# Performance work log

Hardware: AMD Instinct MI355X
Metric: run time of the kernel (lower is better)

## Reference

```python
import jax, jax.numpy as jnp
import numpy as np

N_NODES = 50000
N_EDGES = 800000
NEG_SLOPE = 0.2  # PyG GATConv default


def _gat_layer(x, src, dst, n, W, a_src, a_dst, b, concat):
    """One GATConv layer (PyG semantics, eval mode so attention dropout is off).

    x: [N, F_in], src/dst: [E'] (self loops included), W: [F_in, H*C],
    a_src/a_dst: [H, C], b: [H*C] if concat else [C].
    """
    H, C = a_src.shape
    h = (x @ W).reshape(n, H, C)                      # [N, H, C]
    al_s = jnp.sum(h * a_src, axis=-1)                # [N, H]
    al_d = jnp.sum(h * a_dst, axis=-1)                # [N, H]
    e = jax.nn.leaky_relu(al_s[src] + al_d[dst], NEG_SLOPE)  # [E', H]
    # numerically stable softmax over incoming edges of each dst node
    m = jax.lax.stop_gradient(jax.ops.segment_max(e, dst, num_segments=n))
    m = jnp.where(jnp.isfinite(m), m, 0.0)
    ex = jnp.exp(e - m[dst])                          # [E', H]
    denom = jax.ops.segment_sum(ex, dst, num_segments=n)     # [N, H]
    alpha = ex / denom[dst]                           # safe: self loops => denom > 0
    out = jax.ops.segment_sum(alpha[:, :, None] * h[src], dst, num_segments=n)  # [N,H,C]
    out = out.reshape(n, H * C) if concat else out.mean(axis=1)
    return out + b


def setup_inputs() -> dict:
    key = jax.random.key(0)
    ks = jax.random.split(key, 8)
    in_dim, hid, heads, out_dim = 256, 32, 8, 16
    x = jax.random.normal(ks[0], (N_NODES, in_dim), dtype=jnp.float32)
    edge_index = jax.random.randint(ks[1], (2, N_EDGES), 0, N_NODES, dtype=jnp.int64)
    s1 = 1.0 / np.sqrt(in_dim)
    s2 = 1.0 / np.sqrt(heads * hid)
    return {
        "x": x,
        "edge_index": edge_index,
        "W1": jax.random.normal(ks[2], (in_dim, heads * hid), dtype=jnp.float32) * s1,
        "a_src1": jax.random.normal(ks[3], (heads, hid), dtype=jnp.float32) * s2,
        "a_dst1": jax.random.normal(ks[4], (heads, hid), dtype=jnp.float32) * s2,
        "b1": jnp.zeros((heads * hid,), dtype=jnp.float32),
        "W2": jax.random.normal(ks[5], (heads * hid, out_dim), dtype=jnp.float32) * s2,
        "a_src2": jax.random.normal(ks[6], (1, out_dim), dtype=jnp.float32) * 0.25,
        "a_dst2": jax.random.normal(ks[7], (1, out_dim), dtype=jnp.float32) * 0.25,
        "b2": jnp.zeros((out_dim,), dtype=jnp.float32),
    }


def reference(x, edge_index, W1, a_src1, a_dst1, b1, W2, a_src2, a_dst2, b2):
    n = x.shape[0]
    loops = jnp.arange(n, dtype=edge_index.dtype)
    src = jnp.concatenate([edge_index[0], loops])  # add_self_loops (PyG default)
    dst = jnp.concatenate([edge_index[1], loops])
    h = jax.nn.relu(_gat_layer(x, src, dst, n, W1, a_src1, a_dst1, b1, concat=True))
    # F.dropout(p=0.5, training=False) -> identity in eval mode
    h = _gat_layer(h, src, dst, n, W2, a_src2, a_dst2, b2, concat=False)
    return jax.nn.log_softmax(h, axis=1)
```

## Files before the change

kernel.cpp:

```cpp
#include <hip/hip_runtime.h>
#include <hip/hip_bf16.h>


#define LRELU(x) ((x) > 0.f ? (x) : 0.2f * (x))

typedef __attribute__((ext_vector_type(8))) short short8;
typedef __attribute__((ext_vector_type(8))) unsigned short ushort8;
typedef __attribute__((ext_vector_type(4))) float f32x4;

__device__ inline unsigned short f2b(float f) {
    __hip_bfloat16 h = __float2bfloat16(f);
    return *reinterpret_cast<unsigned short*>(&h);
}
__device__ inline float b2f(unsigned short u) {
    __hip_bfloat16 h;
    *reinterpret_cast<unsigned short*>(&h) = u;
    return __bfloat162float(h);
}


__global__ __launch_bounds__(256) void k_prep(const int* __restrict__ dst, int* deg, int E,
                                              const float* __restrict__ W1,
                                              unsigned short* __restrict__ W1t,
                                              const float* __restrict__ W2,
                                              unsigned short* __restrict__ W2t,
                                              int HB) {
    int b = blockIdx.x, t = threadIdx.x;
    if (b < HB) {
        int i = b * 256 + t;
        if (i < E) atomicAdd(&deg[dst[i]], 1);
    } else if (b < HB + 256) {
        int k = b - HB;
        W1t[t * 256 + k] = f2b(W1[k * 256 + t]);
    } else {
        int nn = b - HB - 256;
        W2t[nn * 256 + t] = f2b(W2[t * 16 + nn]);
    }
}


__global__ __launch_bounds__(256) void k_scanA(const int* __restrict__ deg,
                                               int* __restrict__ tmp,
                                               int* __restrict__ blocksum, int n) {
    __shared__ int sc[256];
    int b = blockIdx.x, t = threadIdx.x;
    int i = b * 256 + t;
    int v = (i < n) ? deg[i] + 1 : 0;
    sc[t] = v;
    __syncthreads();
    for (int off = 1; off < 256; off <<= 1) {
        int x = 0;
        if (t >= off) x = sc[t - off];
        __syncthreads();
        sc[t] += x;
        __syncthreads();
    }
    if (i < n) tmp[i] = sc[t] - v;
    if (t == 255) blocksum[b] = sc[255];
}


__global__ __launch_bounds__(256) void k_scanC(const int* __restrict__ tmp,
                                               const int* __restrict__ blocksum,
                                               int* __restrict__ offs,
                                               int* __restrict__ cursor,
                                               int n, int P, int nb) {
    __shared__ int sc[256];
    __shared__ int base;
    int b = blockIdx.x, t = threadIdx.x;
    int v = (t < nb) ? blocksum[t] : 0;
    sc[t] = v;
    __syncthreads();
    for (int off = 1; off < 256; off <<= 1) {
        int x = 0;
        if (t >= off) x = sc[t - off];
        __syncthreads();
        sc[t] += x;
        __syncthreads();
    }
    if (t == 0) base = (b == 0) ? 0 : sc[b - 1];
    __syncthreads();
    int i = b * 256 + t;
    if (i < n) {
        int o = tmp[i] + base;
        offs[i] = o;
        cursor[i] = o;
    }
    if (b == 0 && t == 0) offs[n] = P;
}

__global__ void k_scatter(const int* __restrict__ src, const int* __restrict__ dst,
                          int* cursor, int* __restrict__ csr, int E, int n) {
    int i = blockIdx.x * blockDim.x + threadIdx.x;
    int s, d;
    if (i < E) {
        s = src[i];
        d = dst[i];
    } else if (i < E + n) {
        s = i - E;
        d = s;
    } else {
        return;
    }
    int p = atomicAdd(&cursor[d], 1);
    csr[p] = s;
}


__global__ __launch_bounds__(256) void k_gemm1(const float* __restrict__ A,
                                               const unsigned short* __restrict__ Wt,
                                               unsigned short* __restrict__ h1b,
                                               const float* __restrict__ asrc,
                                               const float* __restrict__ adst,
                                               float* __restrict__ als,
                                               float* __restrict__ ald, int M) {
    __shared__ unsigned short As[128][40];
    __shared__ unsigned short Bs[128][40];
    int t = threadIdx.x;
    int r0 = blockIdx.x * 128, c0 = blockIdx.y * 128;
    int srow = t >> 1, shalf = t & 1;
    int lane = t & 63, w = t >> 6;
    int lane15 = lane & 15, quad = lane >> 4;
    int rbw = (w & 1) * 64, cbw = (w >> 1) * 64;

    f32x4 acc[4][4];
#pragma unroll
    for (int i = 0; i < 4; i++)
#pragma unroll
        for (int j = 0; j < 4; j++) acc[i][j] = (f32x4)0.f;

    for (int k0 = 0; k0 < 256; k0 += 32) {
        {
            int row = r0 + srow;
            ushort8 p0, p1;
            if (row < M) {
                const float4* sp = (const float4*)&A[(size_t)row * 256 + k0 + shalf * 16];
                float4 f0 = sp[0], f1 = sp[1], f2 = sp[2], f3 = sp[3];
                p0[0] = f2b(f0.x); p0[1] = f2b(f0.y); p0[2] = f2b(f0.z); p0[3] = f2b(f0.w);
                p0[4] = f2b(f1.x); p0[5] = f2b(f1.y); p0[6] = f2b(f1.z); p0[7] = f2b(f1.w);
                p1[0] = f2b(f2.x); p1[1] = f2b(f2.y); p1[2] = f2b(f2.z); p1[3] = f2b(f2.w);
                p1[4] = f2b(f3.x); p1[5] = f2b(f3.y); p1[6] = f2b(f3.z); p1[7] = f2b(f3.w);
            } else {
                p0 = (ushort8)0; p1 = (ushort8)0;
            }
            *(ushort8*)&As[srow][shalf * 16] = p0;
            *(ushort8*)&As[srow][shalf * 16 + 8] = p1;
            const ushort8* bp = (const ushort8*)&Wt[(size_t)(c0 + srow) * 256 + k0 + shalf * 16];
            *(ushort8*)&Bs[srow][shalf * 16] = bp[0];
            *(ushort8*)&Bs[srow][shalf * 16 + 8] = bp[1];
        }
        __syncthreads();
        short8 af[4], bf[4];
#pragma unroll
        for (int i = 0; i < 4; i++)
            af[i] = *(const short8*)&As[rbw + i * 16 + lane15][quad * 8];
#pragma unroll
        for (int j = 0; j < 4; j++)
            bf[j] = *(const short8*)&Bs[cbw + j * 16 + lane15][quad * 8];
#pragma unroll
        for (int i = 0; i < 4; i++)
#pragma unroll
            for (int j = 0; j < 4; j++)
                acc[i][j] = __builtin_amdgcn_mfma_f32_16x16x32_bf16(af[i], bf[j], acc[i][j], 0, 0, 0);
        __syncthreads();
    }

    float asv[4], adv[4];
#pragma unroll
    for (int j = 0; j < 4; j++) {
        asv[j] = asrc[c0 + cbw + j * 16 + lane15];
        adv[j] = adst[c0 + cbw + j * 16 + lane15];
    }
    int hb = (c0 + cbw) >> 5;
#pragma unroll
    for (int i = 0; i < 4; i++) {
        int rowb = r0 + rbw + i * 16 + quad * 4;
#pragma unroll
        for (int j = 0; j < 4; j++) {
            int col = c0 + cbw + j * 16 + lane15;
#pragma unroll
            for (int r = 0; r < 4; r++) {
                int row = rowb + r;
                if (row < M) h1b[(size_t)row * 256 + col] = f2b(acc[i][j][r]);
            }
        }
#pragma unroll
        for (int m = 0; m < 2; m++) {
#pragma unroll
            for (int r = 0; r < 4; r++) {
                float ps = acc[i][2 * m][r] * asv[2 * m] + acc[i][2 * m + 1][r] * asv[2 * m + 1];
                float pd = acc[i][2 * m][r] * adv[2 * m] + acc[i][2 * m + 1][r] * adv[2 * m + 1];
#pragma unroll
                for (int off = 1; off < 16; off <<= 1) {
                    ps += __shfl_xor(ps, off, 16);
                    pd += __shfl_xor(pd, off, 16);
                }
                int row = rowb + r;
                if (lane15 == 0 && row < M) {
                    als[(size_t)row * 8 + hb + m] = ps;
                    ald[(size_t)row * 8 + hb + m] = pd;
                }
            }
        }
    }
}


__global__ __launch_bounds__(128) void k_agg1(const int* __restrict__ csr,
                                              const int* __restrict__ offs,
                                              const float* __restrict__ als,
                                              const float* __restrict__ aldg,
                                              const unsigned short* __restrict__ h1b,
                                              const float* __restrict__ b1,
                                              unsigned short* __restrict__ x2b) {
    int v = blockIdx.x;
    int t = threadIdx.x;
    int start = offs[v];
    int deg = offs[v + 1] - start;
    __shared__ float aldv[8];
    __shared__ int su[32];
    __shared__ float ws[8 * 33];
    if (t < 8) aldv[t] = aldg[v * 8 + t];
    __syncthreads();
    int h = t >> 4;
    const unsigned int* __restrict__ hbase = (const unsigned int*)h1b;
    float a0 = 0.f, a1 = 0.f, wsum = 0.f;
    for (int base = 0; base < deg; base += 32) {
        int cnt = min(32, deg - base);
        int cnt4 = (cnt + 3) & ~3;
        if (base) __syncthreads();
        if (t < cnt4) {
            if (t < cnt) {
                int u = csr[start + base + t];
                su[t] = u;
                const float4* ap = (const float4*)(als + (size_t)u * 8);
                float4 x0 = ap[0], x1 = ap[1];
                ws[0 * 33 + t] = __expf(LRELU(x0.x + aldv[0]));
                ws[1 * 33 + t] = __expf(LRELU(x0.y + aldv[1]));
                ws[2 * 33 + t] = __expf(LRELU(x0.z + aldv[2]));
                ws[3 * 33 + t] = __expf(LRELU(x0.w + aldv[3]));
                ws[4 * 33 + t] = __expf(LRELU(x1.x + aldv[4]));
                ws[5 * 33 + t] = __expf(LRELU(x1.y + aldv[5]));
                ws[6 * 33 + t] = __expf(LRELU(x1.z + aldv[6]));
                ws[7 * 33 + t] = __expf(LRELU(x1.w + aldv[7]));
            } else {
                su[t] = v;
#pragma unroll
                for (int k = 0; k < 8; k++) ws[k * 33 + t] = 0.f;
            }
        }
        __syncthreads();
        for (int e = 0; e < cnt4; e += 4) {
            int u0 = su[e + 0], u1 = su[e + 1], u2 = su[e + 2], u3 = su[e + 3];
            float w0 = ws[h * 33 + e + 0];
            float w1 = ws[h * 33 + e + 1];
            float w2 = ws[h * 33 + e + 2];
            float w3 = ws[h * 33 + e + 3];
            unsigned int pk0 = hbase[u0 * 128 + t];
            unsigned int pk1 = hbase[u1 * 128 + t];
            unsigned int pk2 = hbase[u2 * 128 + t];
            unsigned int pk3 = hbase[u3 * 128 + t];
            a0 += w0 * __uint_as_float(pk0 << 16);
            a1 += w0 * __uint_as_float(pk0 & 0xffff0000u);
            a0 += w1 * __uint_as_float(pk1 << 16);
            a1 += w1 * __uint_as_float(pk1 & 0xffff0000u);
            a0 += w2 * __uint_as_float(pk2 << 16);
            a1 += w2 * __uint_as_float(pk2 & 0xffff0000u);
            a0 += w3 * __uint_as_float(pk3 << 16);
            a1 += w3 * __uint_as_float(pk3 & 0xffff0000u);
            wsum += (w0 + w1) + (w2 + w3);
        }
    }
    const float2* b1v = (const float2*)b1;
    float2 bb = b1v[t];
    float inv = 1.0f / wsum;
    float o0 = a0 * inv + bb.x;
    float o1 = a1 * inv + bb.y;
    o0 = o0 > 0.f ? o0 : 0.f;
    o1 = o1 > 0.f ? o1 : 0.f;
    unsigned int opk = (unsigned int)f2b(o0) | ((unsigned int)f2b(o1) << 16);
    ((unsigned int*)(x2b + (size_t)v * 256))[t] = opk;
}


__global__ __launch_bounds__(256) void k_gemm2(const unsigned short* __restrict__ Xb,
                                               const unsigned short* __restrict__ W2t,
                                               const float* __restrict__ asrc,
                                               const float* __restrict__ adst,
                                               unsigned short* __restrict__ h2b,
                                               float* __restrict__ als,
                                               float* __restrict__ ald, int n) {
    int t = threadIdx.x;
    int lane = t & 63, w = t >> 6;
    int lane15 = lane & 15, quad = lane >> 4;
    int row0 = blockIdx.x * 64 + w * 16;
    f32x4 acc = (f32x4)0.f;
#pragma unroll
    for (int k0 = 0; k0 < 256; k0 += 32) {
        short8 a = *(const short8*)&Xb[(size_t)(row0 + lane15) * 256 + k0 + quad * 8];
        short8 b = *(const short8*)&W2t[lane15 * 256 + k0 + quad * 8];
        acc = __builtin_amdgcn_mfma_f32_16x16x32_bf16(a, b, acc, 0, 0, 0);
    }
    float asv = asrc[lane15], adv = adst[lane15];
#pragma unroll
    for (int r = 0; r < 4; r++) {
        int row = row0 + quad * 4 + r;
        float hv = acc[r];
        float ps = hv * asv, pd = hv * adv;
#pragma unroll
        for (int off = 1; off < 16; off <<= 1) {
            ps += __shfl_xor(ps, off, 16);
            pd += __shfl_xor(pd, off, 16);
        }
        if (row < n) {
            h2b[(size_t)row * 16 + lane15] = f2b(hv);
            if (lane15 == 0) {
                als[row] = ps;
                ald[row] = pd;
            }
        }
    }
}


__global__ __launch_bounds__(256) void k_agg2(const int* __restrict__ csr,
                                              const int* __restrict__ offs,
                                              const float* __restrict__ als,
                                              const float* __restrict__ aldg,
                                              const unsigned short* __restrict__ h2b,
                                              const float* __restrict__ b2,
                                              float* __restrict__ out, int n) {
    int v = blockIdx.x * 4 + (threadIdx.x >> 6);
    if (v >= n) return;
    int lane = threadIdx.x & 63;
    int start = offs[v];
    int deg = offs[v + 1] - start;
    float aldv = aldg[v];
    int c = lane & 15, q = lane >> 4;
    float acc = 0.f, wsum = 0.f;
    for (int e = q; e < deg; e += 4) {
        int u = csr[start + e];
        float x = als[u] + aldv;
        float wv = __expf(LRELU(x));
        acc += wv * b2f(h2b[(size_t)u * 16 + c]);
        wsum += wv;
    }
    acc += __shfl_xor(acc, 32, 64);
    acc += __shfl_xor(acc, 16, 64);
    wsum += __shfl_xor(wsum, 32, 64);
    wsum += __shfl_xor(wsum, 16, 64);
    float o = acc / wsum + b2[c];
    float mx = o;
#pragma unroll
    for (int off = 8; off; off >>= 1) mx = fmaxf(mx, __shfl_xor(mx, off, 16));
    float s = __expf(o - mx);
#pragma unroll
    for (int off = 8; off; off >>= 1) s += __shfl_xor(s, off, 16);
    float res = o - mx - __logf(s);
    if (q == 0) out[(size_t)v * 16 + c] = res;
}


extern "C" void kernel_launch(void* const* d_in, const int* in_sizes, int n_in,
                              void* d_out, int out_size, void* d_ws, size_t ws_size,
                              hipStream_t stream) {
    const float* x = (const float*)d_in[0];
    const int* ei = (const int*)d_in[1];
    const float* W1 = (const float*)d_in[2];
    const float* asrc1 = (const float*)d_in[3];
    const float* adst1 = (const float*)d_in[4];
    const float* b1 = (const float*)d_in[5];
    const float* W2 = (const float*)d_in[6];
    const float* asrc2 = (const float*)d_in[7];
    const float* adst2 = (const float*)d_in[8];
    const float* b2 = (const float*)d_in[9];
    float* out = (float*)d_out;

    int n = in_sizes[0] / 256;
    int E = in_sizes[1] / 2;
    int P = E + n;
    const int* src = ei;
    const int* dst = ei + E;
    int NB = (n + 255) / 256;
    int HB = (E + 255) / 256;

    char* p = (char*)d_ws;
    auto alloc = [&](size_t bytes) {
        void* r = (void*)p;
        p += (bytes + 255) & ~(size_t)255;
        return r;
    };
    unsigned short* h1b = (unsigned short*)alloc((size_t)n * 256 * 2);
    unsigned short* x2b = (unsigned short*)alloc((size_t)n * 256 * 2);
    unsigned short* W1t = (unsigned short*)alloc((size_t)256 * 256 * 2);
    unsigned short* W2t = (unsigned short*)alloc((size_t)16 * 256 * 2);
    float* als1 = (float*)alloc((size_t)n * 8 * 4);
    float* ald1 = (float*)alloc((size_t)n * 8 * 4);
    unsigned short* h2b = (unsigned short*)alloc((size_t)n * 16 * 2);
    float* als2 = (float*)alloc((size_t)n * 4);
    float* ald2 = (float*)alloc((size_t)n * 4);
    int* deg = (int*)alloc((size_t)n * 4);
    int* offs = (int*)alloc((size_t)(n + 1) * 4);
    int* cursor = (int*)alloc((size_t)n * 4);
    int* stmp = (int*)alloc((size_t)n * 4);
    int* blocksum = (int*)alloc((size_t)NB * 4);
    int* csr = (int*)alloc((size_t)P * 4);

    hipMemsetAsync(deg, 0, (size_t)n * 4, stream);
    k_prep<<<HB + 256 + 16, 256, 0, stream>>>(dst, deg, E, W1, W1t, W2, W2t, HB);
    k_scanA<<<NB, 256, 0, stream>>>(deg, stmp, blocksum, n);
    k_scanC<<<NB, 256, 0, stream>>>(stmp, blocksum, offs, cursor, n, P, NB);
    k_scatter<<<(P + 255) / 256, 256, 0, stream>>>(src, dst, cursor, csr, E, n);

    k_gemm1<<<dim3((n + 127) / 128, 2), 256, 0, stream>>>(x, W1t, h1b, asrc1, adst1, als1, ald1, n);
    k_agg1<<<n, 128, 0, stream>>>(csr, offs, als1, ald1, h1b, b1, x2b);

    k_gemm2<<<(n + 63) / 64, 256, 0, stream>>>(x2b, W2t, asrc2, adst2, h2b, als2, ald2, n);
    k_agg2<<<(n + 3) / 4, 256, 0, stream>>>(csr, offs, als2, ald2, h2b, b2, out, n);
}
```

Measured before the change: 340.0 us.

## Pre-convert x to bf16 in prep kernel and fuse CSR scatter into GEMM1 launch

Moves the fp32-to-bf16 conversion of x out of the GEMM1 tile loader into extra blocks of the prep kernel, so GEMM1 loads half as many bytes per A tile. Merges the CSR scatter kernel into the GEMM1 launch as extra blocks, letting the atomic scatter run alongside the matrix multiply and removing one launch. The cost is an extra n×256 bf16 buffer that is written and then read back, which adds memory traffic overall, plus a 2D grid flattened into a combined 1D grid.

```diff
diff --git a/kernel.cpp b/kernel.cpp
--- a/kernel.cpp
+++ b/kernel.cpp
@@ -24,7 +24,9 @@
                                               unsigned short* __restrict__ W1t,
                                               const float* __restrict__ W2,
                                               unsigned short* __restrict__ W2t,
-                                              int HB) {
+                                              const float* __restrict__ x,
+                                              unsigned short* __restrict__ xb,
+                                              int NX, int HB) {
     int b = blockIdx.x, t = threadIdx.x;
     if (b < HB) {
         int i = b * 256 + t;
@@ -32,9 +34,19 @@
     } else if (b < HB + 256) {
         int k = b - HB;
         W1t[t * 256 + k] = f2b(W1[k * 256 + t]);
-    } else {
+    } else if (b < HB + 256 + 16) {
         int nn = b - HB - 256;
         W2t[nn * 256 + t] = f2b(W2[t * 16 + nn]);
+    } else {
+        int i = ((b - HB - 272) * 256 + t) * 8;
+        if (i < NX) {
+            const float4* sp = (const float4*)(x + i);
+            float4 f0 = sp[0], f1 = sp[1];
+            ushort8 o;
+            o[0] = f2b(f0.x); o[1] = f2b(f0.y); o[2] = f2b(f0.z); o[3] = f2b(f0.w);
+            o[4] = f2b(f1.x); o[5] = f2b(f1.y); o[6] = f2b(f1.z); o[7] = f2b(f1.w);
+            *(ushort8*)(xb + i) = o;
+        }
     }
 }
 
@@ -89,35 +101,38 @@
     if (b == 0 && t == 0) offs[n] = P;
 }
 
-__global__ void k_scatter(const int* __restrict__ src, const int* __restrict__ dst,
-                          int* cursor, int* __restrict__ csr, int E, int n) {
-    int i = blockIdx.x * blockDim.x + threadIdx.x;
-    int s, d;
-    if (i < E) {
-        s = src[i];
-        d = dst[i];
-    } else if (i < E + n) {
-        s = i - E;
-        d = s;
-    } else {
-        return;
-    }
-    int p = atomicAdd(&cursor[d], 1);
-    csr[p] = s;
-}
-
-
-__global__ __launch_bounds__(256) void k_gemm1(const float* __restrict__ A,
-                                               const unsigned short* __restrict__ Wt,
-                                               unsigned short* __restrict__ h1b,
-                                               const float* __restrict__ asrc,
-                                               const float* __restrict__ adst,
-                                               float* __restrict__ als,
-                                               float* __restrict__ ald, int M) {
+
+__global__ __launch_bounds__(256) void k_g1sc(const unsigned short* __restrict__ Ab,
+                                              const unsigned short* __restrict__ Wt,
+                                              unsigned short* __restrict__ h1b,
+                                              const float* __restrict__ asrc,
+                                              const float* __restrict__ adst,
+                                              float* __restrict__ als,
+                                              float* __restrict__ ald, int M, int GB,
+                                              const int* __restrict__ src,
+                                              const int* __restrict__ dstv,
+                                              int* cursor, int* __restrict__ csr, int E) {
     __shared__ unsigned short As[128][40];
     __shared__ unsigned short Bs[128][40];
     int t = threadIdx.x;
-    int r0 = blockIdx.x * 128, c0 = blockIdx.y * 128;
+    int b = blockIdx.x;
+    if (b >= GB) {
+        int i = (b - GB) * 256 + t;
+        int s, d;
+        if (i < E) {
+            s = src[i];
+            d = dstv[i];
+        } else if (i < E + M) {
+            s = i - E;
+            d = s;
+        } else {
+            return;
+        }
+        int p = atomicAdd(&cursor[d], 1);
+        csr[p] = s;
+        return;
+    }
+    int r0 = (b >> 1) * 128, c0 = (b & 1) * 128;
     int srow = t >> 1, shalf = t & 1;
     int lane = t & 63, w = t >> 6;
     int lane15 = lane & 15, quad = lane >> 4;
@@ -134,12 +149,9 @@
             int row = r0 + srow;
             ushort8 p0, p1;
             if (row < M) {
-                const float4* sp = (const float4*)&A[(size_t)row * 256 + k0 + shalf * 16];
-                float4 f0 = sp[0], f1 = sp[1], f2 = sp[2], f3 = sp[3];
-                p0[0] = f2b(f0.x); p0[1] = f2b(f0.y); p0[2] = f2b(f0.z); p0[3] = f2b(f0.w);
-                p0[4] = f2b(f1.x); p0[5] = f2b(f1.y); p0[6] = f2b(f1.z); p0[7] = f2b(f1.w);
-                p1[0] = f2b(f2.x); p1[1] = f2b(f2.y); p1[2] = f2b(f2.z); p1[3] = f2b(f2.w);
-                p1[4] = f2b(f3.x); p1[5] = f2b(f3.y); p1[6] = f2b(f3.z); p1[7] = f2b(f3.w);
+                const ushort8* ap = (const ushort8*)&Ab[(size_t)row * 256 + k0 + shalf * 16];
+                p0 = ap[0];
+                p1 = ap[1];
             } else {
                 p0 = (ushort8)0; p1 = (ushort8)0;
             }
@@ -383,6 +395,10 @@
     const int* dst = ei + E;
     int NB = (n + 255) / 256;
     int HB = (E + 255) / 256;
+    int NX = n * 256;
+    int XB = (NX + 2047) / 2048;
+    int GB = ((n + 127) / 128) * 2;
+    int SB = (P + 255) / 256;
 
     char* p = (char*)d_ws;
     auto alloc = [&](size_t bytes) {
@@ -392,6 +408,7 @@
     };
     unsigned short* h1b = (unsigned short*)alloc((size_t)n * 256 * 2);
     unsigned short* x2b = (unsigned short*)alloc((size_t)n * 256 * 2);
+    unsigned short* xb = (unsigned short*)alloc((size_t)n * 256 * 2);
     unsigned short* W1t = (unsigned short*)alloc((size_t)256 * 256 * 2);
     unsigned short* W2t = (unsigned short*)alloc((size_t)16 * 256 * 2);
     float* als1 = (float*)alloc((size_t)n * 8 * 4);
@@ -407,12 +424,12 @@
     int* csr = (int*)alloc((size_t)P * 4);
 
     hipMemsetAsync(deg, 0, (size_t)n * 4, stream);
-    k_prep<<<HB + 256 + 16, 256, 0, stream>>>(dst, deg, E, W1, W1t, W2, W2t, HB);
+    k_prep<<<HB + 272 + XB, 256, 0, stream>>>(dst, deg, E, W1, W1t, W2, W2t, x, xb, NX, HB);
     k_scanA<<<NB, 256, 0, stream>>>(deg, stmp, blocksum, n);
     k_scanC<<<NB, 256, 0, stream>>>(stmp, blocksum, offs, cursor, n, P, NB);
-    k_scatter<<<(P + 255) / 256, 256, 0, stream>>>(src, dst, cursor, csr, E, n);
-
-    k_gemm1<<<dim3((n + 127) / 128, 2), 256, 0, stream>>>(x, W1t, h1b, asrc1, adst1, als1, ald1, n);
+
+    k_g1sc<<<GB + SB, 256, 0, stream>>>(xb, W1t, h1b, asrc1, adst1, als1, ald1, n, GB,
+                                        src, dst, cursor, csr, E);
     k_agg1<<<n, 128, 0, stream>>>(csr, offs, als1, ald1, h1b, b1, x2b);
 
     k_gemm2<<<(n + 63) / 64, 256, 0, stream>>>(x2b, W2t, asrc2, adst2, h2b, als2, ald2, n);
```

Measured after the change: 341.2 us. Within noise of the previous version (+0.4%).
